# Performance work log

Measured on AMD Instinct MI355X. Metric: run time of the kernel, lower is better.

The kernel has to match this reference:

```python
import jax, jax.numpy as jnp
import numpy as np

B, S, D, H = 2, 4096, 512, 8
DK = D // H  # 64

def setup_inputs() -> dict:
    key = jax.random.key(0)
    k1, k2, k3, k4 = jax.random.split(key, 4)
    return {
        "queries": jax.random.normal(k1, (B, S, D), dtype=jnp.float32),
        "keys": jax.random.normal(k2, (B, S, D), dtype=jnp.float32),
        "values": jax.random.normal(k3, (B, S, D), dtype=jnp.float32),
        "W_o": jax.random.normal(k4, (D, D), dtype=jnp.float32) * (1.0 / np.sqrt(D)),
        "b_o": jnp.zeros((D,), dtype=jnp.float32),
    }

def reference(queries, keys, values, W_o, b_o):
    b_s, nq, _ = queries.shape
    nk = keys.shape[1]
    # split heads: (b, s, h, dk) -> (b, h, s, dk)
    q = queries.reshape(b_s, nq, H, DK).transpose(0, 2, 1, 3)
    k = keys.reshape(b_s, nk, H, DK).transpose(0, 2, 1, 3)
    v = values.reshape(b_s, nk, H, DK).transpose(0, 2, 1, 3)
    # full (nq, nk) attention matrix, scaled by sqrt(d_k)
    att = jnp.einsum("bhqd,bhkd->bhqk", q, k) / np.sqrt(DK).astype(np.float32)
    att = jax.nn.softmax(att, axis=-1)  # dropout is identity at inference
    out = jnp.einsum("bhqk,bhkd->bhqd", att, v)
    out = out.transpose(0, 2, 1, 3).reshape(b_s, nq, H * DK)
    return out @ W_o + b_o
```

## Files before the change

kernel.cpp:

```cpp
#include <hip/hip_runtime.h>
#include <hip/hip_bf16.h>

#define Bn 2
#define Sn 4096
#define Dn 512
#define Hn 8

typedef _Float16 f16x8 __attribute__((ext_vector_type(8)));
typedef __fp16 fp16x2 __attribute__((ext_vector_type(2)));
typedef float f32x16 __attribute__((ext_vector_type(16)));
typedef unsigned uint2v __attribute__((ext_vector_type(2)));

#if __has_builtin(__builtin_amdgcn_global_load_lds)
#define HAS_GLL 1
typedef const __attribute__((address_space(1))) unsigned int* gas1_t;
typedef __attribute__((address_space(3))) unsigned int* las3_t;
static __device__ __forceinline__ void ld_lds16(const void* g, void* l) {
    __builtin_amdgcn_global_load_lds((gas1_t)g, (las3_t)l, 16, 0, 0);
}
#else
#define HAS_GLL 0
#endif

static __device__ __forceinline__ unsigned pkh(float a, float b) {
    union { fp16x2 h; unsigned u; } r;
    r.h = __builtin_amdgcn_cvt_pkrtz(a, b);
    return r.u;
}

static __device__ __forceinline__ f16x8 xchg2(unsigned g0x, unsigned g0y,
                                              unsigned g1x, unsigned g1y, int hi) {
    union { unsigned u[4]; f16x8 v; } f;
#if __has_builtin(__builtin_amdgcn_permlane32_swap)
    uint2v rx = __builtin_amdgcn_permlane32_swap(g0x, g1x, false, false);
    uint2v ry = __builtin_amdgcn_permlane32_swap(g0y, g1y, false, false);
    f.u[0] = rx.x; f.u[1] = ry.x; f.u[2] = rx.y; f.u[3] = ry.y;
#else
    int sx = hi ? (int)g0x : (int)g1x;
    int sy = hi ? (int)g0y : (int)g1y;
    int rx = __shfl_xor(sx, 32);
    int ry = __shfl_xor(sy, 32);
    unsigned ox = hi ? g1x : g0x;
    unsigned oy = hi ? g1y : g0y;
    f.u[0] = hi ? (unsigned)rx : ox;
    f.u[1] = hi ? (unsigned)ry : oy;
    f.u[2] = hi ? ox : (unsigned)rx;
    f.u[3] = hi ? oy : (unsigned)ry;
#endif
    return f.v;
}

__global__ __launch_bounds__(256) void prep_kernel(
    const float* __restrict__ K, const float* __restrict__ V, const float* __restrict__ W,
    unsigned short* __restrict__ Kb, unsigned short* __restrict__ Vb,
    unsigned short* __restrict__ Wb) {
    const int vb = blockIdx.x;
    const int tid = threadIdx.x;
    if (vb < 1024) {
        const int kt = vb & 63, bh = vb >> 6;
        const int b = bh >> 3, h = bh & 7;
        unsigned short* dst = Kb + ((size_t)bh * 64 + kt) * 4096;
#pragma unroll
        for (int i = 0; i < 2; ++i) {
            int c = tid + i * 256;
            int f = c >> 6, ln = c & 63;
            int ktile = f >> 2, ks = f & 3;
            int row = ktile * 32 + (ln & 31);
            int dk = ks * 16 + (ln >> 5) * 8;
            const float* src = K + ((size_t)(b * Sn + kt * 64 + row)) * Dn + h * 64 + dk;
            float4 a0 = *(const float4*)src;
            float4 a1 = *(const float4*)(src + 4);
            uint4 o;
            o.x = pkh(a0.x, a0.y); o.y = pkh(a0.z, a0.w);
            o.z = pkh(a1.x, a1.y); o.w = pkh(a1.z, a1.w);
            *(uint4*)(dst + c * 8) = o;
        }
    } else if (vb < 2048) {
        const int u = vb - 1024;
        const int kt = u & 63, bh = u >> 6;
        const int b = bh >> 3, h = bh & 7;
        unsigned short* dst = Vb + ((size_t)bh * 64 + kt) * 4096;
#pragma unroll
        for (int i = 0; i < 2; ++i) {
            int c = tid + i * 256;
            int f = c >> 6, ln = c & 63;
            int dt = f >> 2, ks = f & 3;
            int dk = dt * 32 + (ln & 31);
            int key0 = ks * 16 + (ln >> 5) * 8;
            const float* src = V + ((size_t)(b * Sn + kt * 64 + key0)) * Dn + h * 64 + dk;
            uint4 o;
            o.x = pkh(src[0 * Dn], src[1 * Dn]);
            o.y = pkh(src[2 * Dn], src[3 * Dn]);
            o.z = pkh(src[4 * Dn], src[5 * Dn]);
            o.w = pkh(src[6 * Dn], src[7 * Dn]);
            *(uint4*)(dst + c * 8) = o;
        }
    } else {
        int c = (vb - 2048) * 256 + tid;
        int ln = c & 63, f = c >> 6;
        int ntile = f >> 5, ks = f & 31;
        int n = ntile * 32 + (ln & 31);
        int k0 = ks * 16 + (ln >> 5) * 8;
        uint4 o;
        o.x = pkh(W[(size_t)(k0 + 0) * Dn + n], W[(size_t)(k0 + 1) * Dn + n]);
        o.y = pkh(W[(size_t)(k0 + 2) * Dn + n], W[(size_t)(k0 + 3) * Dn + n]);
        o.z = pkh(W[(size_t)(k0 + 4) * Dn + n], W[(size_t)(k0 + 5) * Dn + n]);
        o.w = pkh(W[(size_t)(k0 + 6) * Dn + n], W[(size_t)(k0 + 7) * Dn + n]);
        *(uint4*)(Wb + c * 8) = o;
    }
}

__global__ __launch_bounds__(512, 4) void attn_kernel(
    const float* __restrict__ Q,
    const unsigned short* __restrict__ Kb,
    const unsigned short* __restrict__ Vb,
    unsigned short* __restrict__ ObA) {
    __shared__ __align__(16) unsigned short KV[32768];

    const int qt = blockIdx.x;
    const int bh = blockIdx.y;
    const int b = bh >> 3, h = bh & 7;
    const int tid = threadIdx.x;
    const int wg = tid >> 6;
    const int half = wg >> 2;
    const int w4 = wg & 3;
    const int lane = tid & 63;
    const int q = lane & 31;
    const int hi = lane >> 5;
    const int q0 = qt * 128 + w4 * 32;
    const float cexp = 0.18033688f;

    f16x8 qf[4];
    {
        const float* qp = Q + ((size_t)(b * Sn + q0 + q)) * Dn + h * 64 + hi * 8;
#pragma unroll
        for (int ks = 0; ks < 4; ++ks) {
            float4 a0 = *(const float4*)(qp + ks * 16);
            float4 a1 = *(const float4*)(qp + ks * 16 + 4);
            union { unsigned u[4]; f16x8 v; } f;
            f.u[0] = pkh(a0.x * cexp, a0.y * cexp);
            f.u[1] = pkh(a0.z * cexp, a0.w * cexp);
            f.u[2] = pkh(a1.x * cexp, a1.y * cexp);
            f.u[3] = pkh(a1.z * cexp, a1.w * cexp);
            qf[ks] = f.v;
        }
    }

    f32x16 zf;
#pragma unroll
    for (int r = 0; r < 16; ++r) zf[r] = 0.f;
    f32x16 oacc[2];
    oacc[0] = zf; oacc[1] = zf;
    float l_ = 0.f;

    const size_t tbase = ((size_t)bh * 64 + half * 32) * 4096;
    const unsigned short* kgw = Kb + tbase + w4 * 1024;
    const unsigned short* vgw = Vb + tbase + w4 * 1024;
    const int lK = half * 4096 + w4 * 1024;
    const int lV = 8192 + half * 4096 + w4 * 1024;

#if HAS_GLL
#define STAGE(itx, bb) { \
    const unsigned short* ksp = kgw + (size_t)(itx) * 4096 + lane * 8; \
    const unsigned short* vsp = vgw + (size_t)(itx) * 4096 + lane * 8; \
    unsigned short* lk = &KV[(bb) * 16384 + lK]; \
    unsigned short* lv = &KV[(bb) * 16384 + lV]; \
    ld_lds16(ksp, lk); ld_lds16(ksp + 512, lk + 512); \
    ld_lds16(vsp, lv); ld_lds16(vsp + 512, lv + 512); }
    STAGE(0, 0);
#else
    const int th = tid & 255;
#define STAGE(itx, bb) { \
    const unsigned short* ksp = kgw - (size_t)w4 * 1024 + (size_t)(itx) * 4096; \
    const unsigned short* vsp = vgw - (size_t)w4 * 1024 + (size_t)(itx) * 4096; \
    uint4 a0 = *(const uint4*)(ksp + th * 8); \
    uint4 a1 = *(const uint4*)(ksp + 2048 + th * 8); \
    uint4 a2 = *(const uint4*)(vsp + th * 8); \
    uint4 a3 = *(const uint4*)(vsp + 2048 + th * 8); \
    unsigned short* lk = &KV[(bb) * 16384 + half * 4096]; \
    unsigned short* lv = &KV[(bb) * 16384 + 8192 + half * 4096]; \
    *(uint4*)&lk[th * 8] = a0; *(uint4*)&lk[2048 + th * 8] = a1; \
    *(uint4*)&lv[th * 8] = a2; *(uint4*)&lv[2048 + th * 8] = a3; }
    STAGE(0, 0);
#endif

    for (int it = 0; it < 32; ++it) {
        __syncthreads();
        const unsigned short* Kbuf = KV + (it & 1) * 16384 + half * 4096;
        const unsigned short* Vbuf = Kbuf + 8192;
        if (it < 31) STAGE(it + 1, (it + 1) & 1);

        f32x16 sa0, sa1;
        {
            f16x8 ka = *(const f16x8*)&Kbuf[0 * 512 + lane * 8];
            f16x8 kb = *(const f16x8*)&Kbuf[4 * 512 + lane * 8];
            sa0 = __builtin_amdgcn_mfma_f32_32x32x16_f16(ka, qf[0], zf, 0, 0, 0);
            sa1 = __builtin_amdgcn_mfma_f32_32x32x16_f16(kb, qf[0], zf, 0, 0, 0);
#pragma unroll
            for (int ks = 1; ks < 4; ++ks) {
                ka = *(const f16x8*)&Kbuf[(0 + ks) * 512 + lane * 8];
                kb = *(const f16x8*)&Kbuf[(4 + ks) * 512 + lane * 8];
                sa0 = __builtin_amdgcn_mfma_f32_32x32x16_f16(ka, qf[ks], sa0, 0, 0, 0);
                sa1 = __builtin_amdgcn_mfma_f32_32x32x16_f16(kb, qf[ks], sa1, 0, 0, 0);
            }
        }
        float e0[16], e1[16];
        float s0 = 0.f, s1 = 0.f;
#pragma unroll
        for (int r = 0; r < 16; ++r) { e0[r] = __builtin_amdgcn_exp2f(sa0[r]); s0 += e0[r]; }
#pragma unroll
        for (int r = 0; r < 16; ++r) { e1[r] = __builtin_amdgcn_exp2f(sa1[r]); s1 += e1[r]; }
        l_ += s0 + s1;

#pragma unroll
        for (int kp = 0; kp < 4; ++kp) {
            const float* e = (kp < 2) ? e0 : e1;
            const int s2 = kp & 1;
            unsigned g0x = pkh(e[8 * s2 + 0], e[8 * s2 + 1]);
            unsigned g0y = pkh(e[8 * s2 + 2], e[8 * s2 + 3]);
            unsigned g1x = pkh(e[8 * s2 + 4], e[8 * s2 + 5]);
            unsigned g1y = pkh(e[8 * s2 + 6], e[8 * s2 + 7]);
            f16x8 pb = xchg2(g0x, g0y, g1x, g1y, hi);
            f16x8 va0 = *(const f16x8*)&Vbuf[(0 + kp) * 512 + lane * 8];
            f16x8 va1 = *(const f16x8*)&Vbuf[(4 + kp) * 512 + lane * 8];
            oacc[0] = __builtin_amdgcn_mfma_f32_32x32x16_f16(va0, pb, oacc[0], 0, 0, 0);
            oacc[1] = __builtin_amdgcn_mfma_f32_32x32x16_f16(va1, pb, oacc[1], 0, 0, 0);
        }
    }

    __syncthreads();
    float* rp = (float*)KV + w4 * 2048;
    float* Ls = (float*)KV + 8192 + w4 * 64;
    if (half) {
#pragma unroll
        for (int g = 0; g < 8; ++g) {
            float4 v;
            v.x = oacc[g >> 2][(g & 3) * 4 + 0];
            v.y = oacc[g >> 2][(g & 3) * 4 + 1];
            v.z = oacc[g >> 2][(g & 3) * 4 + 2];
            v.w = oacc[g >> 2][(g & 3) * 4 + 3];
            *(float4*)&rp[g * 256 + lane * 4] = v;
        }
        Ls[lane] = l_;
    }
    __syncthreads();
    if (!half) {
#pragma unroll
        for (int g = 0; g < 8; ++g) {
            float4 v = *(const float4*)&rp[g * 256 + lane * 4];
            oacc[g >> 2][(g & 3) * 4 + 0] += v.x;
            oacc[g >> 2][(g & 3) * 4 + 1] += v.y;
            oacc[g >> 2][(g & 3) * 4 + 2] += v.z;
            oacc[g >> 2][(g & 3) * 4 + 3] += v.w;
        }
        l_ += Ls[lane];
        l_ += __shfl_xor(l_, 32);
        const float li = 1.f / l_;
        const int gm = b * 128 + qt * 4 + w4;
#pragma unroll
        for (int ksg = 0; ksg < 4; ++ksg) {
            const int dt = ksg >> 1, k2 = ksg & 1;
            unsigned g0x = pkh(oacc[dt][8 * k2 + 0] * li, oacc[dt][8 * k2 + 1] * li);
            unsigned g0y = pkh(oacc[dt][8 * k2 + 2] * li, oacc[dt][8 * k2 + 3] * li);
            unsigned g1x = pkh(oacc[dt][8 * k2 + 4] * li, oacc[dt][8 * k2 + 5] * li);
            unsigned g1y = pkh(oacc[dt][8 * k2 + 6] * li, oacc[dt][8 * k2 + 7] * li);
            f16x8 frag = xchg2(g0x, g0y, g1x, g1y, hi);
            union { f16x8 v; uint4 u; } fu; fu.v = frag;
            *(uint4*)&ObA[((size_t)(gm * 32 + h * 4 + ksg) * 64 + lane) * 8] = fu.u;
        }
    }
}

__global__ __launch_bounds__(256) void proj_kernel(
    const unsigned short* __restrict__ ObA,
    const unsigned short* __restrict__ Wb,
    const float* __restrict__ bias,
    float* __restrict__ out) {
    __shared__ __align__(16) unsigned short Ash[8192];
    __shared__ __align__(16) unsigned short Wsh[4096];

    const int mt = blockIdx.x;
    const int nt = blockIdx.y;
    const int tid = threadIdx.x;
    const int w = tid >> 6;
    const int lane = tid & 63;
    const int q = lane & 31;
    const int hi = lane >> 5;

    f32x16 acc[2];
#pragma unroll
    for (int t = 0; t < 2; ++t)
#pragma unroll
        for (int r = 0; r < 16; ++r) acc[t][r] = 0.f;

    for (int kt = 0; kt < 8; ++kt) {
        __syncthreads();
#pragma unroll
        for (int i = 0; i < 4; ++i) {
            int ci = (tid >> 6) + i * 4;
            int ml = ci >> 2, ksl = ci & 3;
            *(uint4*)&Ash[ci * 512 + lane * 8] =
                *(const uint4*)(ObA + (((size_t)(mt * 4 + ml) * 32 + kt * 4 + ksl) * 64 + lane) * 8);
        }
#pragma unroll
        for (int i = 0; i < 2; ++i) {
            int ci = (tid >> 6) + i * 4;
            int ntl = ci >> 2, ksl = ci & 3;
            *(uint4*)&Wsh[ci * 512 + lane * 8] =
                *(const uint4*)(Wb + (((size_t)(nt * 2 + ntl) * 32 + kt * 4 + ksl) * 64 + lane) * 8);
        }
        __syncthreads();

#pragma unroll
        for (int ks = 0; ks < 4; ++ks) {
            f16x8 a  = *(const f16x8*)&Ash[(w * 4 + ks) * 512 + lane * 8];
            f16x8 b0 = *(const f16x8*)&Wsh[(0 * 4 + ks) * 512 + lane * 8];
            f16x8 b1 = *(const f16x8*)&Wsh[(4 + ks) * 512 + lane * 8];
            acc[0] = __builtin_amdgcn_mfma_f32_32x32x16_f16(a, b0, acc[0], 0, 0, 0);
            acc[1] = __builtin_amdgcn_mfma_f32_32x32x16_f16(a, b1, acc[1], 0, 0, 0);
        }
    }

#pragma unroll
    for (int ntl = 0; ntl < 2; ++ntl) {
        int col = nt * 64 + ntl * 32 + q;
        float bv = bias[col];
#pragma unroll
        for (int reg = 0; reg < 16; ++reg) {
            int row = mt * 128 + w * 32 + (reg & 3) + 8 * (reg >> 2) + 4 * hi;
            out[(size_t)row * Dn + col] = acc[ntl][reg] + bv;
        }
    }
}

extern "C" void kernel_launch(void* const* d_in, const int* in_sizes, int n_in,
                              void* d_out, int out_size, void* d_ws, size_t ws_size,
                              hipStream_t stream) {
    const float* Q = (const float*)d_in[0];
    const float* K = (const float*)d_in[1];
    const float* V = (const float*)d_in[2];
    const float* W = (const float*)d_in[3];
    const float* bo = (const float*)d_in[4];
    float* out = (float*)d_out;

    char* ws = (char*)d_ws;
    unsigned short* Kb  = (unsigned short*)(ws);
    unsigned short* Vb  = (unsigned short*)(ws + 8388608);
    unsigned short* Wb  = (unsigned short*)(ws + 16777216);
    unsigned short* ObA = (unsigned short*)(ws + 17301504);

    prep_kernel<<<2176, 256, 0, stream>>>(K, V, W, Kb, Vb, Wb);
    attn_kernel<<<dim3(32, 16), 512, 0, stream>>>(Q, Kb, Vb, ObA);
    proj_kernel<<<dim3(64, 8), 256, 0, stream>>>(ObA, Wb, bo, out);
}
```

Before: 181.9 us.

## Drop KV split across half-blocks and software-pipeline PV MFMA with next tile

The attention block shrinks from 512 to 256 threads. Each wave now walks all 64 key tiles itself, so the LDS reduction that merged the two key halves at the end is gone. The loop is software-pipelined: the P·V MFMAs for the previous tile run after the next tile's barrier and staging, overlapping them with the QK and exp work of the current tile. Each block does twice as many serial iterations and keeps extra registers for the V and P fragments, and the grid size is unchanged, so there are fewer waves per CU.

```diff
diff --git a/kernel.cpp b/kernel.cpp
--- a/kernel.cpp
+++ b/kernel.cpp
@@ -110,24 +110,22 @@
     }
 }
 
-__global__ __launch_bounds__(512, 4) void attn_kernel(
+__global__ __launch_bounds__(256, 2) void attn_kernel(
     const float* __restrict__ Q,
     const unsigned short* __restrict__ Kb,
     const unsigned short* __restrict__ Vb,
     unsigned short* __restrict__ ObA) {
-    __shared__ __align__(16) unsigned short KV[32768];
+    __shared__ __align__(16) unsigned short KV[16384];
 
     const int qt = blockIdx.x;
     const int bh = blockIdx.y;
     const int b = bh >> 3, h = bh & 7;
     const int tid = threadIdx.x;
-    const int wg = tid >> 6;
-    const int half = wg >> 2;
-    const int w4 = wg & 3;
+    const int w = tid >> 6;
     const int lane = tid & 63;
     const int q = lane & 31;
     const int hi = lane >> 5;
-    const int q0 = qt * 128 + w4 * 32;
+    const int q0 = qt * 128 + w * 32;
     const float cexp = 0.18033688f;
 
     f16x8 qf[4];
@@ -153,43 +151,39 @@
     oacc[0] = zf; oacc[1] = zf;
     float l_ = 0.f;
 
-    const size_t tbase = ((size_t)bh * 64 + half * 32) * 4096;
-    const unsigned short* kgw = Kb + tbase + w4 * 1024;
-    const unsigned short* vgw = Vb + tbase + w4 * 1024;
-    const int lK = half * 4096 + w4 * 1024;
-    const int lV = 8192 + half * 4096 + w4 * 1024;
+    f16x8 va[8];
+    f16x8 pb[4];
+
+    const size_t tbase = (size_t)bh * 64 * 4096;
+    const unsigned short* kgw = Kb + tbase + w * 1024;
+    const unsigned short* vgw = Vb + tbase + w * 1024;
+    const int lK = w * 1024;
+    const int lV = 4096 + w * 1024;
 
 #if HAS_GLL
 #define STAGE(itx, bb) { \
     const unsigned short* ksp = kgw + (size_t)(itx) * 4096 + lane * 8; \
     const unsigned short* vsp = vgw + (size_t)(itx) * 4096 + lane * 8; \
-    unsigned short* lk = &KV[(bb) * 16384 + lK]; \
-    unsigned short* lv = &KV[(bb) * 16384 + lV]; \
+    unsigned short* lk = &KV[(bb) * 8192 + lK]; \
+    unsigned short* lv = &KV[(bb) * 8192 + lV]; \
     ld_lds16(ksp, lk); ld_lds16(ksp + 512, lk + 512); \
     ld_lds16(vsp, lv); ld_lds16(vsp + 512, lv + 512); }
-    STAGE(0, 0);
 #else
-    const int th = tid & 255;
 #define STAGE(itx, bb) { \
-    const unsigned short* ksp = kgw - (size_t)w4 * 1024 + (size_t)(itx) * 4096; \
-    const unsigned short* vsp = vgw - (size_t)w4 * 1024 + (size_t)(itx) * 4096; \
-    uint4 a0 = *(const uint4*)(ksp + th * 8); \
-    uint4 a1 = *(const uint4*)(ksp + 2048 + th * 8); \
-    uint4 a2 = *(const uint4*)(vsp + th * 8); \
-    uint4 a3 = *(const uint4*)(vsp + 2048 + th * 8); \
-    unsigned short* lk = &KV[(bb) * 16384 + half * 4096]; \
-    unsigned short* lv = &KV[(bb) * 16384 + 8192 + half * 4096]; \
-    *(uint4*)&lk[th * 8] = a0; *(uint4*)&lk[2048 + th * 8] = a1; \
-    *(uint4*)&lv[th * 8] = a2; *(uint4*)&lv[2048 + th * 8] = a3; }
-    STAGE(0, 0);
+    const unsigned short* ksp = Kb + tbase + (size_t)(itx) * 4096; \
+    const unsigned short* vsp = Vb + tbase + (size_t)(itx) * 4096; \
+    uint4 a0 = *(const uint4*)(ksp + tid * 8); \
+    uint4 a1 = *(const uint4*)(ksp + 2048 + tid * 8); \
+    uint4 a2 = *(const uint4*)(vsp + tid * 8); \
+    uint4 a3 = *(const uint4*)(vsp + 2048 + tid * 8); \
+    unsigned short* lk = &KV[(bb) * 8192]; \
+    unsigned short* lv = lk + 4096; \
+    *(uint4*)&lk[tid * 8] = a0; *(uint4*)&lk[2048 + tid * 8] = a1; \
+    *(uint4*)&lv[tid * 8] = a2; *(uint4*)&lv[2048 + tid * 8] = a3; }
 #endif
 
-    for (int it = 0; it < 32; ++it) {
-        __syncthreads();
-        const unsigned short* Kbuf = KV + (it & 1) * 16384 + half * 4096;
-        const unsigned short* Vbuf = Kbuf + 8192;
-        if (it < 31) STAGE(it + 1, (it + 1) & 1);
-
+    auto TILE = [&](const unsigned short* Kbuf) {
+        const unsigned short* Vbuf = Kbuf + 4096;
         f32x16 sa0, sa1;
         {
             f16x8 ka = *(const f16x8*)&Kbuf[0 * 512 + lane * 8];
@@ -211,7 +205,6 @@
 #pragma unroll
         for (int r = 0; r < 16; ++r) { e1[r] = __builtin_amdgcn_exp2f(sa1[r]); s1 += e1[r]; }
         l_ += s0 + s1;
-
 #pragma unroll
         for (int kp = 0; kp < 4; ++kp) {
             const float* e = (kp < 2) ? e0 : e1;
@@ -220,54 +213,48 @@
             unsigned g0y = pkh(e[8 * s2 + 2], e[8 * s2 + 3]);
             unsigned g1x = pkh(e[8 * s2 + 4], e[8 * s2 + 5]);
             unsigned g1y = pkh(e[8 * s2 + 6], e[8 * s2 + 7]);
-            f16x8 pb = xchg2(g0x, g0y, g1x, g1y, hi);
-            f16x8 va0 = *(const f16x8*)&Vbuf[(0 + kp) * 512 + lane * 8];
-            f16x8 va1 = *(const f16x8*)&Vbuf[(4 + kp) * 512 + lane * 8];
-            oacc[0] = __builtin_amdgcn_mfma_f32_32x32x16_f16(va0, pb, oacc[0], 0, 0, 0);
-            oacc[1] = __builtin_amdgcn_mfma_f32_32x32x16_f16(va1, pb, oacc[1], 0, 0, 0);
-        }
-    }
-
+            pb[kp] = xchg2(g0x, g0y, g1x, g1y, hi);
+        }
+#pragma unroll
+        for (int kp = 0; kp < 4; ++kp) {
+            va[kp]     = *(const f16x8*)&Vbuf[(0 + kp) * 512 + lane * 8];
+            va[4 + kp] = *(const f16x8*)&Vbuf[(4 + kp) * 512 + lane * 8];
+        }
+    };
+
+#define PV() { \
+    _Pragma("unroll") \
+    for (int kp = 0; kp < 4; ++kp) { \
+        oacc[0] = __builtin_amdgcn_mfma_f32_32x32x16_f16(va[kp], pb[kp], oacc[0], 0, 0, 0); \
+        oacc[1] = __builtin_amdgcn_mfma_f32_32x32x16_f16(va[4 + kp], pb[kp], oacc[1], 0, 0, 0); } }
+
+    STAGE(0, 0);
     __syncthreads();
-    float* rp = (float*)KV + w4 * 2048;
-    float* Ls = (float*)KV + 8192 + w4 * 64;
-    if (half) {
-#pragma unroll
-        for (int g = 0; g < 8; ++g) {
-            float4 v;
-            v.x = oacc[g >> 2][(g & 3) * 4 + 0];
-            v.y = oacc[g >> 2][(g & 3) * 4 + 1];
-            v.z = oacc[g >> 2][(g & 3) * 4 + 2];
-            v.w = oacc[g >> 2][(g & 3) * 4 + 3];
-            *(float4*)&rp[g * 256 + lane * 4] = v;
-        }
-        Ls[lane] = l_;
-    }
-    __syncthreads();
-    if (!half) {
-#pragma unroll
-        for (int g = 0; g < 8; ++g) {
-            float4 v = *(const float4*)&rp[g * 256 + lane * 4];
-            oacc[g >> 2][(g & 3) * 4 + 0] += v.x;
-            oacc[g >> 2][(g & 3) * 4 + 1] += v.y;
-            oacc[g >> 2][(g & 3) * 4 + 2] += v.z;
-            oacc[g >> 2][(g & 3) * 4 + 3] += v.w;
-        }
-        l_ += Ls[lane];
-        l_ += __shfl_xor(l_, 32);
-        const float li = 1.f / l_;
-        const int gm = b * 128 + qt * 4 + w4;
-#pragma unroll
-        for (int ksg = 0; ksg < 4; ++ksg) {
-            const int dt = ksg >> 1, k2 = ksg & 1;
-            unsigned g0x = pkh(oacc[dt][8 * k2 + 0] * li, oacc[dt][8 * k2 + 1] * li);
-            unsigned g0y = pkh(oacc[dt][8 * k2 + 2] * li, oacc[dt][8 * k2 + 3] * li);
-            unsigned g1x = pkh(oacc[dt][8 * k2 + 4] * li, oacc[dt][8 * k2 + 5] * li);
-            unsigned g1y = pkh(oacc[dt][8 * k2 + 6] * li, oacc[dt][8 * k2 + 7] * li);
-            f16x8 frag = xchg2(g0x, g0y, g1x, g1y, hi);
-            union { f16x8 v; uint4 u; } fu; fu.v = frag;
-            *(uint4*)&ObA[((size_t)(gm * 32 + h * 4 + ksg) * 64 + lane) * 8] = fu.u;
-        }
+    STAGE(1, 1);
+    TILE(&KV[0]);
+
+    for (int it = 1; it < 64; ++it) {
+        __syncthreads();
+        if (it < 63) STAGE(it + 1, (it + 1) & 1);
+        const unsigned short* Kbuf = &KV[(it & 1) * 8192];
+        PV();
+        TILE(Kbuf);
+    }
+    PV();
+
+    l_ += __shfl_xor(l_, 32);
+    const float li = 1.f / l_;
+    const int gm = b * 128 + qt * 4 + w;
+#pragma unroll
+    for (int ksg = 0; ksg < 4; ++ksg) {
+        const int dt = ksg >> 1, k2 = ksg & 1;
+        unsigned g0x = pkh(oacc[dt][8 * k2 + 0] * li, oacc[dt][8 * k2 + 1] * li);
+        unsigned g0y = pkh(oacc[dt][8 * k2 + 2] * li, oacc[dt][8 * k2 + 3] * li);
+        unsigned g1x = pkh(oacc[dt][8 * k2 + 4] * li, oacc[dt][8 * k2 + 5] * li);
+        unsigned g1y = pkh(oacc[dt][8 * k2 + 6] * li, oacc[dt][8 * k2 + 7] * li);
+        f16x8 frag = xchg2(g0x, g0y, g1x, g1y, hi);
+        union { f16x8 v; uint4 u; } fu; fu.v = frag;
+        *(uint4*)&ObA[((size_t)(gm * 32 + h * 4 + ksg) * 64 + lane) * 8] = fu.u;
     }
 }
 
@@ -350,6 +337,6 @@
     unsigned short* ObA = (unsigned short*)(ws + 17301504);
 
     prep_kernel<<<2176, 256, 0, stream>>>(K, V, W, Kb, Vb, Wb);
-    attn_kernel<<<dim3(32, 16), 512, 0, stream>>>(Q, Kb, Vb, ObA);
+    attn_kernel<<<dim3(32, 16), 256, 0, stream>>>(Q, Kb, Vb, ObA);
     proj_kernel<<<dim3(64, 8), 256, 0, stream>>>(ObA, Wb, bo, out);
 }
```

Measured after the change: 184.3 us. About the same (+1.3%).

## Load K fragments directly from global, stage only V in LDS, swizzle blocks

Applied to the files above, without the earlier changes.

K tiles are no longer staged through shared memory; each lane loads its MFMA K fragments directly from global memory (relying on L2 since the four q-tile waves share them), while only V stays double-buffered in LDS. This halves LDS usage, which may allow more resident blocks, and removes the LDS write/read round trip for K. The block index is also remapped so consecutive blocks cover different heads within the same q-tile group, changing L2 locality. The risk is exposed global latency on K loads inside the loop with no prefetch, plus redundant K fetches across waves.

```diff
diff --git a/kernel.cpp b/kernel.cpp
--- a/kernel.cpp
+++ b/kernel.cpp
@@ -115,10 +115,11 @@
     const unsigned short* __restrict__ Kb,
     const unsigned short* __restrict__ Vb,
     unsigned short* __restrict__ ObA) {
-    __shared__ __align__(16) unsigned short KV[32768];
-
-    const int qt = blockIdx.x;
-    const int bh = blockIdx.y;
+    __shared__ __align__(16) unsigned short Vs[17408];
+
+    const int id = blockIdx.x + (blockIdx.y << 5);
+    const int qt = (id >> 3) & 31;
+    const int bh = (id & 7) + ((id >> 8) << 3);
     const int b = bh >> 3, h = bh & 7;
     const int tid = threadIdx.x;
     const int wg = tid >> 6;
@@ -154,56 +155,52 @@
     float l_ = 0.f;
 
     const size_t tbase = ((size_t)bh * 64 + half * 32) * 4096;
-    const unsigned short* kgw = Kb + tbase + w4 * 1024;
+    const unsigned short* kg = Kb + tbase + lane * 8;
     const unsigned short* vgw = Vb + tbase + w4 * 1024;
-    const int lK = half * 4096 + w4 * 1024;
-    const int lV = 8192 + half * 4096 + w4 * 1024;
+    const int lV = half * 4096 + w4 * 1024;
 
 #if HAS_GLL
-#define STAGE(itx, bb) { \
-    const unsigned short* ksp = kgw + (size_t)(itx) * 4096 + lane * 8; \
+#define STAGE_V(itx, bb) { \
     const unsigned short* vsp = vgw + (size_t)(itx) * 4096 + lane * 8; \
-    unsigned short* lk = &KV[(bb) * 16384 + lK]; \
-    unsigned short* lv = &KV[(bb) * 16384 + lV]; \
-    ld_lds16(ksp, lk); ld_lds16(ksp + 512, lk + 512); \
+    unsigned short* lv = &Vs[(bb) * 8192 + lV]; \
     ld_lds16(vsp, lv); ld_lds16(vsp + 512, lv + 512); }
-    STAGE(0, 0);
 #else
     const int th = tid & 255;
-#define STAGE(itx, bb) { \
-    const unsigned short* ksp = kgw - (size_t)w4 * 1024 + (size_t)(itx) * 4096; \
+#define STAGE_V(itx, bb) { \
     const unsigned short* vsp = vgw - (size_t)w4 * 1024 + (size_t)(itx) * 4096; \
-    uint4 a0 = *(const uint4*)(ksp + th * 8); \
-    uint4 a1 = *(const uint4*)(ksp + 2048 + th * 8); \
     uint4 a2 = *(const uint4*)(vsp + th * 8); \
     uint4 a3 = *(const uint4*)(vsp + 2048 + th * 8); \
-    unsigned short* lk = &KV[(bb) * 16384 + half * 4096]; \
-    unsigned short* lv = &KV[(bb) * 16384 + 8192 + half * 4096]; \
-    *(uint4*)&lk[th * 8] = a0; *(uint4*)&lk[2048 + th * 8] = a1; \
+    unsigned short* lv = &Vs[(bb) * 8192 + half * 4096]; \
     *(uint4*)&lv[th * 8] = a2; *(uint4*)&lv[2048 + th * 8] = a3; }
-    STAGE(0, 0);
 #endif
+
+    STAGE_V(0, 0);
 
     for (int it = 0; it < 32; ++it) {
         __syncthreads();
-        const unsigned short* Kbuf = KV + (it & 1) * 16384 + half * 4096;
-        const unsigned short* Vbuf = Kbuf + 8192;
-        if (it < 31) STAGE(it + 1, (it + 1) & 1);
+        const unsigned short* Vbuf = Vs + (it & 1) * 8192 + half * 4096;
+        if (it < 31) STAGE_V(it + 1, (it + 1) & 1);
+
+        const unsigned short* kp_ = kg + (size_t)it * 4096;
+        f16x8 kf0 = *(const f16x8*)(kp_ + 0 * 512);
+        f16x8 kf1 = *(const f16x8*)(kp_ + 1 * 512);
+        f16x8 kf2 = *(const f16x8*)(kp_ + 2 * 512);
+        f16x8 kf3 = *(const f16x8*)(kp_ + 3 * 512);
+        f16x8 kf4 = *(const f16x8*)(kp_ + 4 * 512);
+        f16x8 kf5 = *(const f16x8*)(kp_ + 5 * 512);
+        f16x8 kf6 = *(const f16x8*)(kp_ + 6 * 512);
+        f16x8 kf7 = *(const f16x8*)(kp_ + 7 * 512);
 
         f32x16 sa0, sa1;
-        {
-            f16x8 ka = *(const f16x8*)&Kbuf[0 * 512 + lane * 8];
-            f16x8 kb = *(const f16x8*)&Kbuf[4 * 512 + lane * 8];
-            sa0 = __builtin_amdgcn_mfma_f32_32x32x16_f16(ka, qf[0], zf, 0, 0, 0);
-            sa1 = __builtin_amdgcn_mfma_f32_32x32x16_f16(kb, qf[0], zf, 0, 0, 0);
-#pragma unroll
-            for (int ks = 1; ks < 4; ++ks) {
-                ka = *(const f16x8*)&Kbuf[(0 + ks) * 512 + lane * 8];
-                kb = *(const f16x8*)&Kbuf[(4 + ks) * 512 + lane * 8];
-                sa0 = __builtin_amdgcn_mfma_f32_32x32x16_f16(ka, qf[ks], sa0, 0, 0, 0);
-                sa1 = __builtin_amdgcn_mfma_f32_32x32x16_f16(kb, qf[ks], sa1, 0, 0, 0);
-            }
-        }
+        sa0 = __builtin_amdgcn_mfma_f32_32x32x16_f16(kf0, qf[0], zf, 0, 0, 0);
+        sa1 = __builtin_amdgcn_mfma_f32_32x32x16_f16(kf4, qf[0], zf, 0, 0, 0);
+        sa0 = __builtin_amdgcn_mfma_f32_32x32x16_f16(kf1, qf[1], sa0, 0, 0, 0);
+        sa1 = __builtin_amdgcn_mfma_f32_32x32x16_f16(kf5, qf[1], sa1, 0, 0, 0);
+        sa0 = __builtin_amdgcn_mfma_f32_32x32x16_f16(kf2, qf[2], sa0, 0, 0, 0);
+        sa1 = __builtin_amdgcn_mfma_f32_32x32x16_f16(kf6, qf[2], sa1, 0, 0, 0);
+        sa0 = __builtin_amdgcn_mfma_f32_32x32x16_f16(kf3, qf[3], sa0, 0, 0, 0);
+        sa1 = __builtin_amdgcn_mfma_f32_32x32x16_f16(kf7, qf[3], sa1, 0, 0, 0);
+
         float e0[16], e1[16];
         float s0 = 0.f, s1 = 0.f;
 #pragma unroll
@@ -229,8 +226,8 @@
     }
 
     __syncthreads();
-    float* rp = (float*)KV + w4 * 2048;
-    float* Ls = (float*)KV + 8192 + w4 * 64;
+    float* rp = (float*)Vs + w4 * 2048;
+    float* Ls = (float*)Vs + 8192 + w4 * 64;
     if (half) {
 #pragma unroll
         for (int g = 0; g < 8; ++g) {
```

New measurement: 188.7 us. 3.7% more time.

## Give each attention wave two query tiles to reuse K/V fragments

Applied to the files above, without the earlier changes.

Attention blocks shrink from 8 waves to 4, and each wave now handles 64 queries as two 32-row tiles. Each K and V fragment read from LDS is reused for two MFMAs, which halves LDS read traffic per unit of work. Staging is split so one wave loads K and the other loads V per key half. The cost is more accumulator registers per wave (four 32x32 output tiles) and fewer waves per block, which may lower occupancy or latency hiding, and the launch-bounds hint changes to match.

```diff
diff --git a/kernel.cpp b/kernel.cpp
--- a/kernel.cpp
+++ b/kernel.cpp
@@ -110,7 +110,7 @@
     }
 }
 
-__global__ __launch_bounds__(512, 4) void attn_kernel(
+__global__ __launch_bounds__(256, 2) void attn_kernel(
     const float* __restrict__ Q,
     const unsigned short* __restrict__ Kb,
     const unsigned short* __restrict__ Vb,
@@ -122,151 +122,170 @@
     const int b = bh >> 3, h = bh & 7;
     const int tid = threadIdx.x;
     const int wg = tid >> 6;
-    const int half = wg >> 2;
-    const int w4 = wg & 3;
+    const int half = wg >> 1;
+    const int qs = wg & 1;
     const int lane = tid & 63;
     const int q = lane & 31;
     const int hi = lane >> 5;
-    const int q0 = qt * 128 + w4 * 32;
     const float cexp = 0.18033688f;
 
-    f16x8 qf[4];
+    f16x8 qf0[4], qf1[4];
     {
-        const float* qp = Q + ((size_t)(b * Sn + q0 + q)) * Dn + h * 64 + hi * 8;
+        const float* qp0 = Q + ((size_t)(b * Sn + qt * 128 + qs * 64 + q)) * Dn + h * 64 + hi * 8;
+        const float* qp1 = qp0 + (size_t)32 * Dn;
 #pragma unroll
         for (int ks = 0; ks < 4; ++ks) {
-            float4 a0 = *(const float4*)(qp + ks * 16);
-            float4 a1 = *(const float4*)(qp + ks * 16 + 4);
+            float4 a0 = *(const float4*)(qp0 + ks * 16);
+            float4 a1 = *(const float4*)(qp0 + ks * 16 + 4);
             union { unsigned u[4]; f16x8 v; } f;
             f.u[0] = pkh(a0.x * cexp, a0.y * cexp);
             f.u[1] = pkh(a0.z * cexp, a0.w * cexp);
             f.u[2] = pkh(a1.x * cexp, a1.y * cexp);
             f.u[3] = pkh(a1.z * cexp, a1.w * cexp);
-            qf[ks] = f.v;
+            qf0[ks] = f.v;
+            a0 = *(const float4*)(qp1 + ks * 16);
+            a1 = *(const float4*)(qp1 + ks * 16 + 4);
+            f.u[0] = pkh(a0.x * cexp, a0.y * cexp);
+            f.u[1] = pkh(a0.z * cexp, a0.w * cexp);
+            f.u[2] = pkh(a1.x * cexp, a1.y * cexp);
+            f.u[3] = pkh(a1.z * cexp, a1.w * cexp);
+            qf1[ks] = f.v;
         }
     }
 
     f32x16 zf;
 #pragma unroll
     for (int r = 0; r < 16; ++r) zf[r] = 0.f;
-    f32x16 oacc[2];
-    oacc[0] = zf; oacc[1] = zf;
-    float l_ = 0.f;
+    f32x16 oacc[2][2];
+    oacc[0][0] = zf; oacc[0][1] = zf; oacc[1][0] = zf; oacc[1][1] = zf;
+    float l0_ = 0.f, l1_ = 0.f;
 
     const size_t tbase = ((size_t)bh * 64 + half * 32) * 4096;
-    const unsigned short* kgw = Kb + tbase + w4 * 1024;
-    const unsigned short* vgw = Vb + tbase + w4 * 1024;
-    const int lK = half * 4096 + w4 * 1024;
-    const int lV = 8192 + half * 4096 + w4 * 1024;
+    const unsigned short* sgw = (qs ? Vb : Kb) + tbase;
+    unsigned short* const lbase = &KV[half * 8192 + qs * 4096];
 
 #if HAS_GLL
 #define STAGE(itx, bb) { \
-    const unsigned short* ksp = kgw + (size_t)(itx) * 4096 + lane * 8; \
-    const unsigned short* vsp = vgw + (size_t)(itx) * 4096 + lane * 8; \
-    unsigned short* lk = &KV[(bb) * 16384 + lK]; \
-    unsigned short* lv = &KV[(bb) * 16384 + lV]; \
-    ld_lds16(ksp, lk); ld_lds16(ksp + 512, lk + 512); \
-    ld_lds16(vsp, lv); ld_lds16(vsp + 512, lv + 512); }
+    const unsigned short* sp = sgw + (size_t)(itx) * 4096 + lane * 8; \
+    unsigned short* ld = lbase + (bb) * 16384; \
+    _Pragma("unroll") \
+    for (int c = 0; c < 8; ++c) ld_lds16(sp + c * 512, ld + c * 512); }
+#else
+#define STAGE(itx, bb) { \
+    const unsigned short* sp = sgw + (size_t)(itx) * 4096 + lane * 8; \
+    unsigned short* ld = lbase + (bb) * 16384; \
+    _Pragma("unroll") \
+    for (int c = 0; c < 8; ++c) { \
+        uint4 a = *(const uint4*)(sp + c * 512); \
+        *(uint4*)&ld[c * 512 + lane * 8] = a; } }
+#endif
+
     STAGE(0, 0);
-#else
-    const int th = tid & 255;
-#define STAGE(itx, bb) { \
-    const unsigned short* ksp = kgw - (size_t)w4 * 1024 + (size_t)(itx) * 4096; \
-    const unsigned short* vsp = vgw - (size_t)w4 * 1024 + (size_t)(itx) * 4096; \
-    uint4 a0 = *(const uint4*)(ksp + th * 8); \
-    uint4 a1 = *(const uint4*)(ksp + 2048 + th * 8); \
-    uint4 a2 = *(const uint4*)(vsp + th * 8); \
-    uint4 a3 = *(const uint4*)(vsp + 2048 + th * 8); \
-    unsigned short* lk = &KV[(bb) * 16384 + half * 4096]; \
-    unsigned short* lv = &KV[(bb) * 16384 + 8192 + half * 4096]; \
-    *(uint4*)&lk[th * 8] = a0; *(uint4*)&lk[2048 + th * 8] = a1; \
-    *(uint4*)&lv[th * 8] = a2; *(uint4*)&lv[2048 + th * 8] = a3; }
-    STAGE(0, 0);
-#endif
 
     for (int it = 0; it < 32; ++it) {
         __syncthreads();
-        const unsigned short* Kbuf = KV + (it & 1) * 16384 + half * 4096;
-        const unsigned short* Vbuf = Kbuf + 8192;
+        const unsigned short* Kbuf = &KV[(it & 1) * 16384 + half * 8192];
+        const unsigned short* Vbuf = Kbuf + 4096;
         if (it < 31) STAGE(it + 1, (it + 1) & 1);
 
-        f32x16 sa0, sa1;
-        {
-            f16x8 ka = *(const f16x8*)&Kbuf[0 * 512 + lane * 8];
-            f16x8 kb = *(const f16x8*)&Kbuf[4 * 512 + lane * 8];
-            sa0 = __builtin_amdgcn_mfma_f32_32x32x16_f16(ka, qf[0], zf, 0, 0, 0);
-            sa1 = __builtin_amdgcn_mfma_f32_32x32x16_f16(kb, qf[0], zf, 0, 0, 0);
-#pragma unroll
-            for (int ks = 1; ks < 4; ++ks) {
-                ka = *(const f16x8*)&Kbuf[(0 + ks) * 512 + lane * 8];
-                kb = *(const f16x8*)&Kbuf[(4 + ks) * 512 + lane * 8];
-                sa0 = __builtin_amdgcn_mfma_f32_32x32x16_f16(ka, qf[ks], sa0, 0, 0, 0);
-                sa1 = __builtin_amdgcn_mfma_f32_32x32x16_f16(kb, qf[ks], sa1, 0, 0, 0);
-            }
-        }
-        float e0[16], e1[16];
-        float s0 = 0.f, s1 = 0.f;
-#pragma unroll
-        for (int r = 0; r < 16; ++r) { e0[r] = __builtin_amdgcn_exp2f(sa0[r]); s0 += e0[r]; }
-#pragma unroll
-        for (int r = 0; r < 16; ++r) { e1[r] = __builtin_amdgcn_exp2f(sa1[r]); s1 += e1[r]; }
-        l_ += s0 + s1;
-
-#pragma unroll
-        for (int kp = 0; kp < 4; ++kp) {
-            const float* e = (kp < 2) ? e0 : e1;
-            const int s2 = kp & 1;
-            unsigned g0x = pkh(e[8 * s2 + 0], e[8 * s2 + 1]);
-            unsigned g0y = pkh(e[8 * s2 + 2], e[8 * s2 + 3]);
-            unsigned g1x = pkh(e[8 * s2 + 4], e[8 * s2 + 5]);
-            unsigned g1y = pkh(e[8 * s2 + 6], e[8 * s2 + 7]);
-            f16x8 pb = xchg2(g0x, g0y, g1x, g1y, hi);
-            f16x8 va0 = *(const f16x8*)&Vbuf[(0 + kp) * 512 + lane * 8];
-            f16x8 va1 = *(const f16x8*)&Vbuf[(4 + kp) * 512 + lane * 8];
-            oacc[0] = __builtin_amdgcn_mfma_f32_32x32x16_f16(va0, pb, oacc[0], 0, 0, 0);
-            oacc[1] = __builtin_amdgcn_mfma_f32_32x32x16_f16(va1, pb, oacc[1], 0, 0, 0);
+#pragma unroll
+        for (int kt2 = 0; kt2 < 2; ++kt2) {
+            f32x16 sa0, sa1;
+            {
+                f16x8 kf = *(const f16x8*)&Kbuf[(kt2 * 4 + 0) * 512 + lane * 8];
+                sa0 = __builtin_amdgcn_mfma_f32_32x32x16_f16(kf, qf0[0], zf, 0, 0, 0);
+                sa1 = __builtin_amdgcn_mfma_f32_32x32x16_f16(kf, qf1[0], zf, 0, 0, 0);
+#pragma unroll
+                for (int ks = 1; ks < 4; ++ks) {
+                    kf = *(const f16x8*)&Kbuf[(kt2 * 4 + ks) * 512 + lane * 8];
+                    sa0 = __builtin_amdgcn_mfma_f32_32x32x16_f16(kf, qf0[ks], sa0, 0, 0, 0);
+                    sa1 = __builtin_amdgcn_mfma_f32_32x32x16_f16(kf, qf1[ks], sa1, 0, 0, 0);
+                }
+            }
+            unsigned u0[8], u1[8];
+            float s0 = 0.f, s1 = 0.f;
+#pragma unroll
+            for (int j = 0; j < 8; ++j) {
+                float ea = __builtin_amdgcn_exp2f(sa0[2 * j]);
+                float eb = __builtin_amdgcn_exp2f(sa0[2 * j + 1]);
+                s0 += ea + eb;
+                u0[j] = pkh(ea, eb);
+            }
+#pragma unroll
+            for (int j = 0; j < 8; ++j) {
+                float ea = __builtin_amdgcn_exp2f(sa1[2 * j]);
+                float eb = __builtin_amdgcn_exp2f(sa1[2 * j + 1]);
+                s1 += ea + eb;
+                u1[j] = pkh(ea, eb);
+            }
+            l0_ += s0; l1_ += s1;
+
+#pragma unroll
+            for (int kp = 0; kp < 2; ++kp) {
+                f16x8 pb0 = xchg2(u0[4 * kp + 0], u0[4 * kp + 1], u0[4 * kp + 2], u0[4 * kp + 3], hi);
+                f16x8 pb1 = xchg2(u1[4 * kp + 0], u1[4 * kp + 1], u1[4 * kp + 2], u1[4 * kp + 3], hi);
+                f16x8 va0 = *(const f16x8*)&Vbuf[(0 * 4 + kt2 * 2 + kp) * 512 + lane * 8];
+                f16x8 va1 = *(const f16x8*)&Vbuf[(1 * 4 + kt2 * 2 + kp) * 512 + lane * 8];
+                oacc[0][0] = __builtin_amdgcn_mfma_f32_32x32x16_f16(va0, pb0, oacc[0][0], 0, 0, 0);
+                oacc[0][1] = __builtin_amdgcn_mfma_f32_32x32x16_f16(va1, pb0, oacc[0][1], 0, 0, 0);
+                oacc[1][0] = __builtin_amdgcn_mfma_f32_32x32x16_f16(va0, pb1, oacc[1][0], 0, 0, 0);
+                oacc[1][1] = __builtin_amdgcn_mfma_f32_32x32x16_f16(va1, pb1, oacc[1][1], 0, 0, 0);
+            }
         }
     }
 
     __syncthreads();
-    float* rp = (float*)KV + w4 * 2048;
-    float* Ls = (float*)KV + 8192 + w4 * 64;
+    float* red = (float*)KV + qs * 4224;
     if (half) {
 #pragma unroll
-        for (int g = 0; g < 8; ++g) {
-            float4 v;
-            v.x = oacc[g >> 2][(g & 3) * 4 + 0];
-            v.y = oacc[g >> 2][(g & 3) * 4 + 1];
-            v.z = oacc[g >> 2][(g & 3) * 4 + 2];
-            v.w = oacc[g >> 2][(g & 3) * 4 + 3];
-            *(float4*)&rp[g * 256 + lane * 4] = v;
-        }
-        Ls[lane] = l_;
+        for (int t = 0; t < 2; ++t)
+#pragma unroll
+            for (int dt = 0; dt < 2; ++dt)
+#pragma unroll
+                for (int g = 0; g < 4; ++g) {
+                    float4 v;
+                    v.x = oacc[t][dt][g * 4 + 0];
+                    v.y = oacc[t][dt][g * 4 + 1];
+                    v.z = oacc[t][dt][g * 4 + 2];
+                    v.w = oacc[t][dt][g * 4 + 3];
+                    *(float4*)&red[((t * 2 + dt) * 4 + g) * 256 + lane * 4] = v;
+                }
+        red[4096 + lane] = l0_;
+        red[4096 + 64 + lane] = l1_;
     }
     __syncthreads();
     if (!half) {
 #pragma unroll
-        for (int g = 0; g < 8; ++g) {
-            float4 v = *(const float4*)&rp[g * 256 + lane * 4];
-            oacc[g >> 2][(g & 3) * 4 + 0] += v.x;
-            oacc[g >> 2][(g & 3) * 4 + 1] += v.y;
-            oacc[g >> 2][(g & 3) * 4 + 2] += v.z;
-            oacc[g >> 2][(g & 3) * 4 + 3] += v.w;
-        }
-        l_ += Ls[lane];
-        l_ += __shfl_xor(l_, 32);
-        const float li = 1.f / l_;
-        const int gm = b * 128 + qt * 4 + w4;
-#pragma unroll
-        for (int ksg = 0; ksg < 4; ++ksg) {
-            const int dt = ksg >> 1, k2 = ksg & 1;
-            unsigned g0x = pkh(oacc[dt][8 * k2 + 0] * li, oacc[dt][8 * k2 + 1] * li);
-            unsigned g0y = pkh(oacc[dt][8 * k2 + 2] * li, oacc[dt][8 * k2 + 3] * li);
-            unsigned g1x = pkh(oacc[dt][8 * k2 + 4] * li, oacc[dt][8 * k2 + 5] * li);
-            unsigned g1y = pkh(oacc[dt][8 * k2 + 6] * li, oacc[dt][8 * k2 + 7] * li);
-            f16x8 frag = xchg2(g0x, g0y, g1x, g1y, hi);
-            union { f16x8 v; uint4 u; } fu; fu.v = frag;
-            *(uint4*)&ObA[((size_t)(gm * 32 + h * 4 + ksg) * 64 + lane) * 8] = fu.u;
+        for (int t = 0; t < 2; ++t)
+#pragma unroll
+            for (int dt = 0; dt < 2; ++dt)
+#pragma unroll
+                for (int g = 0; g < 4; ++g) {
+                    float4 v = *(const float4*)&red[((t * 2 + dt) * 4 + g) * 256 + lane * 4];
+                    oacc[t][dt][g * 4 + 0] += v.x;
+                    oacc[t][dt][g * 4 + 1] += v.y;
+                    oacc[t][dt][g * 4 + 2] += v.z;
+                    oacc[t][dt][g * 4 + 3] += v.w;
+                }
+        l0_ += red[4096 + lane];
+        l1_ += red[4096 + 64 + lane];
+        l0_ += __shfl_xor(l0_, 32);
+        l1_ += __shfl_xor(l1_, 32);
+#pragma unroll
+        for (int t = 0; t < 2; ++t) {
+            const float li = 1.f / (t ? l1_ : l0_);
+            const int gm = b * 128 + qt * 4 + qs * 2 + t;
+#pragma unroll
+            for (int ksg = 0; ksg < 4; ++ksg) {
+                const int dt = ksg >> 1, k2 = ksg & 1;
+                unsigned g0x = pkh(oacc[t][dt][8 * k2 + 0] * li, oacc[t][dt][8 * k2 + 1] * li);
+                unsigned g0y = pkh(oacc[t][dt][8 * k2 + 2] * li, oacc[t][dt][8 * k2 + 3] * li);
+                unsigned g1x = pkh(oacc[t][dt][8 * k2 + 4] * li, oacc[t][dt][8 * k2 + 5] * li);
+                unsigned g1y = pkh(oacc[t][dt][8 * k2 + 6] * li, oacc[t][dt][8 * k2 + 7] * li);
+                f16x8 frag = xchg2(g0x, g0y, g1x, g1y, hi);
+                union { f16x8 v; uint4 u; } fu; fu.v = frag;
+                *(uint4*)&ObA[((size_t)(gm * 32 + h * 4 + ksg) * 64 + lane) * 8] = fu.u;
+            }
         }
     }
 }
@@ -350,6 +369,6 @@
     unsigned short* ObA = (unsigned short*)(ws + 17301504);
 
     prep_kernel<<<2176, 256, 0, stream>>>(K, V, W, Kb, Vb, Wb);
-    attn_kernel<<<dim3(32, 16), 512, 0, stream>>>(Q, Kb, Vb, ObA);
+    attn_kernel<<<dim3(32, 16), 256, 0, stream>>>(Q, Kb, Vb, ObA);
     proj_kernel<<<dim3(64, 8), 256, 0, stream>>>(ObA, Wb, bo, out);
 }
```

Measured after the change: 178.0 us. -2.1%, faster.
